# Kernel optimization log

Hardware: AMD Instinct MI355X
Metric: run time of the kernel (lower is better)

## Reference

```python
import jax, jax.numpy as jnp
import numpy as np

EPS = 1e-5

def _ln(x, g, b):
    mu = jnp.mean(x, -1, keepdims=True)
    var = jnp.mean((x - mu) ** 2, -1, keepdims=True)
    return (x - mu) / jnp.sqrt(var + EPS) * g + b

def _edge_scores(x, lat, mask, sn_g, sn_b, tn_g, tn_b, su_w, su_b, tp_w, tp_b, m1_w, m1_b, m2_w, m2_b):
    # x: [B,S,D], lat: [B,K,D] -> edges [B,S,K]
    s = _ln(x, sn_g, sn_b) @ su_w + su_b      # [B,S,E]
    t = _ln(lat, tn_g, tn_b) @ tp_w + tp_b    # [B,K,E]
    B, S, E = s.shape
    K = t.shape[1]
    s4 = jnp.broadcast_to(s[:, :, None, :], (B, S, K, E))
    t4 = jnp.broadcast_to(t[:, None, :, :], (B, S, K, E))
    pair = jnp.concatenate([s4, t4, s4 * t4], axis=-1)  # [B,S,K,3E]
    h = jax.nn.gelu(pair @ m1_w + m1_b, approximate=False)
    e = (h @ m2_w + m2_b)[..., 0]             # [B,S,K]
    e = e / (1.0 + jnp.abs(e))                # softsign
    return e * mask[:, :, None]

def setup_inputs() -> dict:
    key = jax.random.key(0)
    B, St, Si, K, D, E = 2, 2048, 1024, 64, 768, 256
    ks = iter(jax.random.split(key, 64))
    d = {}
    d['text_values'] = jax.random.normal(next(ks), (B, St, D), jnp.float32)
    d['image_values'] = jax.random.normal(next(ks), (B, Si, D), jnp.float32)
    d['latent_state_init'] = jax.random.normal(next(ks), (B, K, D), jnp.float32)
    d['latent_value_init'] = jax.random.normal(next(ks), (B, K, D), jnp.float32)
    d['text_mask'] = jnp.ones((B, St), jnp.float32)
    d['image_mask'] = jnp.ones((B, Si), jnp.float32)
    def scorer(prefix):
        d[prefix + 'sn_g'] = jnp.ones((D,), jnp.float32)
        d[prefix + 'sn_b'] = jnp.zeros((D,), jnp.float32)
        d[prefix + 'tn_g'] = jnp.ones((D,), jnp.float32)
        d[prefix + 'tn_b'] = jnp.zeros((D,), jnp.float32)
        d[prefix + 'su_w'] = jax.random.normal(next(ks), (D, E), jnp.float32) * 0.02
        d[prefix + 'su_b'] = jnp.zeros((E,), jnp.float32)
        d[prefix + 'tp_w'] = jax.random.normal(next(ks), (D, E), jnp.float32) * 0.02
        d[prefix + 'tp_b'] = jnp.zeros((E,), jnp.float32)
        d[prefix + 'm1_w'] = jax.random.normal(next(ks), (3 * E, E), jnp.float32) * 0.02
        d[prefix + 'm1_b'] = jnp.zeros((E,), jnp.float32)
        d[prefix + 'm2_w'] = jax.random.normal(next(ks), (E, 1), jnp.float32) * 0.02
        d[prefix + 'm2_b'] = jnp.zeros((1,), jnp.float32)
    scorer('t_')
    scorer('i_')
    for p in ['tsn', 'isn', 'stn', 'vn']:
        d[p + '_g'] = jnp.ones((D,), jnp.float32)
        d[p + '_b'] = jnp.zeros((D,), jnp.float32)
    d['tsp_w'] = jax.random.normal(next(ks), (D, D), jnp.float32) * 0.02
    d['tsp_b'] = jnp.zeros((D,), jnp.float32)
    d['isp_w'] = jax.random.normal(next(ks), (D, D), jnp.float32) * 0.02
    d['isp_b'] = jnp.zeros((D,), jnp.float32)
    return d

def reference(text_values, image_values, latent_state_init, latent_value_init, text_mask, image_mask,
              t_sn_g, t_sn_b, t_tn_g, t_tn_b, t_su_w, t_su_b, t_tp_w, t_tp_b, t_m1_w, t_m1_b, t_m2_w, t_m2_b,
              i_sn_g, i_sn_b, i_tn_g, i_tn_b, i_su_w, i_su_b, i_tp_w, i_tp_b, i_m1_w, i_m1_b, i_m2_w, i_m2_b,
              tsn_g, tsn_b, isn_g, isn_b, stn_g, stn_b, vn_g, vn_b, tsp_w, tsp_b, isp_w, isp_b):
    t2l = _edge_scores(text_values, latent_value_init, text_mask,
                       t_sn_g, t_sn_b, t_tn_g, t_tn_b, t_su_w, t_su_b, t_tp_w, t_tp_b, t_m1_w, t_m1_b, t_m2_w, t_m2_b)
    i2l = _edge_scores(image_values, latent_value_init, image_mask,
                       i_sn_g, i_sn_b, i_tn_g, i_tn_b, i_su_w, i_su_b, i_tp_w, i_tp_b, i_m1_w, i_m1_b, i_m2_w, i_m2_b)
    tsf = _ln(text_values, tsn_g, tsn_b) @ tsp_w + tsp_b    # [B,St,D]
    isf = _ln(image_values, isn_g, isn_b) @ isp_w + isp_b   # [B,Si,D]
    state_raw = jnp.einsum('bsk,bsd->bkd', t2l, tsf) + jnp.einsum('bsk,bsd->bkd', i2l, isf)
    value_raw = jnp.einsum('bsk,bsd->bkd', t2l, text_values) + jnp.einsum('bsk,bsd->bkd', i2l, image_values)
    latent_state = _ln(state_raw + latent_state_init, stn_g, stn_b)
    latent_value = _ln(value_raw + latent_value_init, vn_g, vn_b)
    return latent_state, latent_value, t2l, i2l
```

## Files before the change

### kernel.cpp

```cpp
#include <hip/hip_runtime.h>
#include <math.h>

#define EPS_LN 1e-5f

#define B_  2
#define ST_ 2048
#define SI_ 1024
#define K_  64
#define D_  768
#define E_  256

typedef __bf16 bf16x8 __attribute__((ext_vector_type(8)));
typedef float  f32x4  __attribute__((ext_vector_type(4)));
typedef unsigned short ushort_t;

__device__ inline ushort_t f2bf(float x) {
    unsigned int u = __float_as_uint(x);
    unsigned int r = (u + 0x7FFFu + ((u >> 16) & 1u)) >> 16;
    return (ushort_t)r;
}

__device__ inline float gelu_fast(float z) {
    float x2 = z * z;
    float u = 0.7978845608f * z * fmaf(0.044715f, x2, 1.0f);
    float t = __expf(-2.0f * fabsf(u));
    float r = __builtin_amdgcn_rcpf(1.0f + t);
    float th = fmaf(t * r, -2.0f, 1.0f);
    return fmaf(0.5f * fabsf(z), th, 0.5f * z);
}

__global__ __launch_bounds__(256) void ln_stats_kernel(
    const float* __restrict__ xt, const float* __restrict__ xi,
    const float* __restrict__ xl, float* __restrict__ mu, float* __restrict__ rstd)
{
    int w = threadIdx.x >> 6, lane = threadIdx.x & 63;
    int row = blockIdx.x * 4 + w;
    const float* src;
    if (row < 4096) src = xt + (size_t)row * D_;
    else if (row < 6144) src = xi + (size_t)(row - 4096) * D_;
    else src = xl + (size_t)(row - 6144) * D_;
    float s = 0.f, q = 0.f;
    #pragma unroll
    for (int rep = 0; rep < 3; ++rep) {
        float4 v = *(const float4*)(src + lane * 4 + rep * 256);
        s += v.x + v.y + v.z + v.w;
        q += v.x * v.x + v.y * v.y + v.z * v.z + v.w * v.w;
    }
    #pragma unroll
    for (int off = 32; off > 0; off >>= 1) {
        s += __shfl_xor(s, off, 64);
        q += __shfl_xor(q, off, 64);
    }
    if (lane == 0) {
        float m = s / (float)D_;
        float var = q / (float)D_ - m * m;
        mu[row] = m;
        rstd[row] = rsqrtf(var + EPS_LN);
    }
}

__global__ __launch_bounds__(256) void fold_all_kernel(
    const float* b0, const float* W0, const float* w0, float* f0,
    const float* b1, const float* W1, const float* w1, float* f1,
    const float* b2, const float* W2, const float* w2, float* f2,
    const float* b3, const float* W3, const float* w3, float* f3,
    const float* b4, const float* W4, const float* w4, float* f4,
    const float* b5, const float* W5, const float* w5, float* f5)
{
    const float* blns[6] = {b0, b1, b2, b3, b4, b5};
    const float* Ws[6]   = {W0, W1, W2, W3, W4, W5};
    const float* wbs[6]  = {w0, w1, w2, w3, w4, w5};
    float* bfs[6]        = {f0, f1, f2, f3, f4, f5};
    int cfg = blockIdx.z;
    int E = (cfg >= 4) ? 768 : 256;
    if ((int)blockIdx.x * 64 >= E) return;
    const float* bln = blns[cfg];
    const float* W = Ws[cfg];
    __shared__ float red[4][64];
    int c = threadIdx.x & 63, part = threadIdx.x >> 6;
    int e = blockIdx.x * 64 + c;
    int d0 = blockIdx.y * 64;
    float s = 0.f;
    #pragma unroll
    for (int i = 0; i < 16; ++i) {
        int d = d0 + part * 16 + i;
        s += bln[d] * W[(size_t)d * E + e];
    }
    red[part][c] = s; __syncthreads();
    if (part == 0) {
        float v = red[0][c] + red[1][c] + red[2][c] + red[3][c];
        if (blockIdx.y == 0 && wbs[cfg]) v += wbs[cfg][e];
        atomicAdd(&bfs[cfg][e], v);
    }
}

__global__ __launch_bounds__(256) void tpack_kernel(
    const float* __restrict__ xt, const float* __restrict__ xi,
    const float* __restrict__ mu, const float* __restrict__ rstd,
    ushort_t* __restrict__ XrF_t, ushort_t* __restrict__ XhF_t, ushort_t* __restrict__ AF_t,
    ushort_t* __restrict__ XrF_i, ushort_t* __restrict__ XhF_i, ushort_t* __restrict__ AF_i)
{
    __shared__ float tile[64][65];
    __shared__ float mu_s[64], rs_s[64];
    int bx = blockIdx.x;
    int isImg = bx >= 64;
    const float* x = isImg ? xi : xt;
    ushort_t* XrF = isImg ? XrF_i : XrF_t;
    ushort_t* XhF = isImg ? XhF_i : XhF_t;
    ushort_t* AF  = isImg ? AF_i  : AF_t;
    int rbase = (isImg ? bx - 64 : bx) * 64;
    int statOff = isImg ? 4096 : 0;
    int d0 = blockIdx.y * 64;
    int t = threadIdx.x;
    #pragma unroll
    for (int rep = 0; rep < 4; ++rep) {
        int rl = (t >> 4) + rep * 16;
        int c4 = (t & 15) * 4;
        *(float4*)&tile[rl][c4] = *(const float4*)(x + (size_t)(rbase + rl) * D_ + d0 + c4);
    }
    if (t < 64) { mu_s[t] = mu[statOff + rbase + t]; rs_s[t] = rstd[statOff + rbase + t]; }
    __syncthreads();
    int lane = t & 63;
    #pragma unroll
    for (int rep = 0; rep < 2; ++rep) {
        int idx = t + rep * 256;
        int nt = (idx >> 6) & 3, cl = (idx >> 8) & 1;
        int kl = cl * 32 + (lane >> 4) * 8;
        int nl = nt * 16 + (lane & 15);
        ushort_t orw[8], oh[8];
        #pragma unroll
        for (int j = 0; j < 8; ++j) {
            float v = tile[kl + j][nl];
            orw[j] = f2bf(v);
            oh[j]  = f2bf((v - mu_s[kl + j]) * rs_s[kl + j]);
        }
        size_t chunk = (size_t)((rbase >> 5) + cl);
        size_t o = ((chunk * 48 + (d0 >> 4) + nt) * 64 + lane) * 8;
        *reinterpret_cast<uint4*>(XrF + o) = *reinterpret_cast<uint4*>(orw);
        *reinterpret_cast<uint4*>(XhF + o) = *reinterpret_cast<uint4*>(oh);
    }
    #pragma unroll
    for (int rep = 0; rep < 2; ++rep) {
        int idx = t + rep * 256;
        int cl = (idx >> 6) & 1, tl = idx >> 7;
        int rl = tl * 16 + (lane & 15);
        int dl = cl * 32 + (lane >> 4) * 8;
        float m = mu_s[rl], rs = rs_s[rl];
        ushort_t o8[8];
        #pragma unroll
        for (int j = 0; j < 8; ++j)
            o8[j] = f2bf((tile[rl][dl + j] - m) * rs);
        size_t o = (((size_t)(rbase >> 4) + tl) * 24 + (d0 >> 5) + cl) * 512 + lane * 8;
        *reinterpret_cast<uint4*>(AF + o) = *reinterpret_cast<uint4*>(o8);
    }
}

__global__ __launch_bounds__(256) void packB_kernel(const float* __restrict__ W,
                                                    const float* __restrict__ g,
                                                    ushort_t* __restrict__ out,
                                                    int Kd, int N) {
    int idx = blockIdx.x * 256 + threadIdx.x;
    int nTile = N >> 4;
    int total = (Kd >> 5) * nTile * 64;
    if (idx >= total) return;
    int lane = idx & 63;
    int ntile = (idx >> 6) % nTile;
    int c = idx / (64 * nTile);
    int n = ntile * 16 + (lane & 15);
    int k0 = c * 32 + (lane >> 4) * 8;
    ushort_t o[8];
    #pragma unroll
    for (int j = 0; j < 8; ++j) {
        int k = k0 + j;
        float v = W[(size_t)k * N + n];
        if (g) v *= g[k];
        o[j] = f2bf(v);
    }
    *reinterpret_cast<uint4*>(out + (size_t)idx * 8) = *reinterpret_cast<uint4*>(o);
}

__global__ __launch_bounds__(256) void sgemm_split_kernel(
    const float* A0, const float* B0, const float* rs0, const float* bias0,
    const float* mu0, const float* sd0, int so0, float* C0,
    const float* A1, const float* B1, const float* rs1, const float* bias1,
    const float* mu1, const float* sd1, int so1, float* C1,
    int nz0, int Kd, int N)
{
    int z = blockIdx.z;
    int cfg = (z >= nz0) ? 1 : 0;
    int kz = cfg ? (z - nz0) : z;
    const float* A = cfg ? A1 : A0;
    const float* Bm = cfg ? B1 : B0;
    const float* rowScale = cfg ? rs1 : rs0;
    const float* bias = cfg ? bias1 : bias0;
    const float* muA = cfg ? mu1 : mu0;
    const float* sdA = cfg ? sd1 : sd0;
    int so = cfg ? so1 : so0;
    float* C = cfg ? C1 : C0;

    __shared__ float As[16][65];
    __shared__ float Bs[16][64];
    int tx = threadIdx.x, ty = threadIdx.y;
    int tid = ty * 16 + tx;
    int row0 = blockIdx.y * 64;
    int col0 = blockIdx.x * 64;
    float acc[4][4] = {};
    int kbase = kz * 128;
    for (int k0 = kbase; k0 < kbase + 128; k0 += 16) {
        {
            int e = tid * 4;
            int r = e >> 4, kk = e & 15;
            float4 av = *(const float4*)(A + (size_t)(row0 + r) * Kd + k0 + kk);
            if (muA) {
                float m = muA[so + row0 + r], sd = sdA[so + row0 + r];
                av.x = (av.x - m) * sd; av.y = (av.y - m) * sd;
                av.z = (av.z - m) * sd; av.w = (av.w - m) * sd;
            }
            As[kk + 0][r] = av.x; As[kk + 1][r] = av.y; As[kk + 2][r] = av.z; As[kk + 3][r] = av.w;
        }
        {
            int e = tid * 4;
            int kk = e >> 6, c = e & 63;
            float4 bv = *(const float4*)(Bm + (size_t)(k0 + kk) * N + col0 + c);
            if (rowScale) {
                float sc = rowScale[k0 + kk];
                bv.x *= sc; bv.y *= sc; bv.z *= sc; bv.w *= sc;
            }
            *(float4*)&Bs[kk][c] = bv;
        }
        __syncthreads();
        #pragma unroll
        for (int kk = 0; kk < 16; ++kk) {
            float a[4], b[4];
            #pragma unroll
            for (int i = 0; i < 4; ++i) a[i] = As[kk][ty + 16 * i];
            #pragma unroll
            for (int j = 0; j < 4; ++j) b[j] = Bs[kk][tx + 16 * j];
            #pragma unroll
            for (int i = 0; i < 4; ++i)
                #pragma unroll
                for (int j = 0; j < 4; ++j)
                    acc[i][j] += a[i] * b[j];
        }
        __syncthreads();
    }
    #pragma unroll
    for (int i = 0; i < 4; ++i) {
        int r = row0 + ty + 16 * i;
        #pragma unroll
        for (int j = 0; j < 4; ++j) {
            int c = col0 + tx + 16 * j;
            float v = acc[i][j];
            if (kz == 0 && bias) v += bias[c];
            atomicAdd(&C[(size_t)r * N + c], v);
        }
    }
}

__global__ __launch_bounds__(256) void sproj_mfma_kernel(
    const ushort_t* __restrict__ AF_t, const ushort_t* __restrict__ BF_t,
    const float* __restrict__ bias_t, ushort_t* __restrict__ sF_t,
    const ushort_t* __restrict__ AF_i, const ushort_t* __restrict__ BF_i,
    const float* __restrict__ bias_i, ushort_t* __restrict__ sF_i)
{
    __shared__ __align__(16) ushort_t ls[4][32][72];
    int bx = blockIdx.x;
    int isImg = bx >= 128;
    const ushort_t* AF = isImg ? AF_i : AF_t;
    const ushort_t* BF = isImg ? BF_i : BF_t;
    const float* bias = isImg ? bias_i : bias_t;
    ushort_t* sF = isImg ? sF_i : sF_t;
    int tile0 = (isImg ? bx - 128 : bx) * 2;

    int w = threadIdx.x >> 6, lane = threadIdx.x & 63;
    int quad = lane >> 4, n16 = lane & 15;

    f32x4 acc[2][4];
    #pragma unroll
    for (int mt = 0; mt < 2; ++mt)
        #pragma unroll
        for (int nt = 0; nt < 4; ++nt)
            acc[mt][nt] = (f32x4){0.f, 0.f, 0.f, 0.f};

    for (int c = 0; c < 24; ++c) {
        bf16x8 af[2], bf[4];
        #pragma unroll
        for (int mt = 0; mt < 2; ++mt)
            af[mt] = *reinterpret_cast<const bf16x8*>(AF + ((size_t)(tile0 + mt) * 24 + c) * 512 + lane * 8);
        #pragma unroll
        for (int nt = 0; nt < 4; ++nt)
            bf[nt] = *reinterpret_cast<const bf16x8*>(BF + ((size_t)c * 16 + w * 4 + nt) * 512 + lane * 8);
        #pragma unroll
        for (int mt = 0; mt < 2; ++mt)
            #pragma unroll
            for (int nt = 0; nt < 4; ++nt)
                acc[mt][nt] = __builtin_amdgcn_mfma_f32_16x16x32_bf16(af[mt], bf[nt], acc[mt][nt], 0, 0, 0);
    }
    #pragma unroll
    for (int mt = 0; mt < 2; ++mt)
        #pragma unroll
        for (int nt = 0; nt < 4; ++nt) {
            float bv = bias[w * 64 + nt * 16 + n16];
            #pragma unroll
            for (int r = 0; r < 4; ++r)
                ls[w][mt * 16 + quad * 4 + r][nt * 16 + n16] = f2bf(acc[mt][nt][r] + bv);
        }
    __syncthreads();
    #pragma unroll
    for (int mt = 0; mt < 2; ++mt)
        #pragma unroll
        for (int h = 0; h < 2; ++h) {
            uint4 v = *reinterpret_cast<const uint4*>(&ls[w][mt * 16 + n16][h * 32 + quad * 8]);
            *reinterpret_cast<uint4*>(sF + ((size_t)(tile0 + mt) * 8 + 2 * w + h) * 512 + lane * 8) = v;
        }
}

__global__ __launch_bounds__(256) void pack_M_kernel(
    const float* __restrict__ tP_t, const float* __restrict__ W3_t,
    const float* __restrict__ W1_t, ushort_t* __restrict__ MF_t,
    const float* __restrict__ tP_i, const float* __restrict__ W3_i,
    const float* __restrict__ W1_i, ushort_t* __restrict__ MF_i)
{
    const int HALF = B_ * K_ * 16 * 8 * 64;
    int gidx = blockIdx.x * 256 + threadIdx.x;
    int isImg = gidx >= HALF;
    int idx = isImg ? gidx - HALF : gidx;
    const float* tP = isImg ? tP_i : tP_t;
    const float* W3 = isImg ? W3_i : W3_t;
    const float* W1 = isImg ? W1_i : W1_t;
    ushort_t* MF = isImg ? MF_i : MF_t;
    int lane = idx & 63;
    int kc = (idx >> 6) & 7;
    int nt = (idx >> 9) & 15;
    int bk = idx >> 13;
    int n = nt * 16 + (lane & 15);
    int e0 = kc * 32 + (lane >> 4) * 8;
    ushort_t out[8];
    #pragma unroll
    for (int j = 0; j < 8; ++j) {
        int e = e0 + j;
        float v = tP[(size_t)bk * E_ + e] * W3[(size_t)e * E_ + n] + W1[(size_t)e * E_ + n];
        out[j] = f2bf(v);
    }
    *reinterpret_cast<uint4*>(MF + (size_t)idx * 8) = *reinterpret_cast<uint4*>(out);
}

__global__ __launch_bounds__(256, 4) void cross_mfma_kernel(
    const ushort_t* __restrict__ sF_t, const ushort_t* __restrict__ MF_t,
    const float* __restrict__ c2_t, const float* __restrict__ m2w_t,
    const float* __restrict__ m2b_t, const float* __restrict__ mask_t,
    float* __restrict__ out_t,
    const ushort_t* __restrict__ sF_i, const ushort_t* __restrict__ MF_i,
    const float* __restrict__ c2_i, const float* __restrict__ m2w_i,
    const float* __restrict__ m2b_i, const float* __restrict__ mask_i,
    float* __restrict__ out_i)
{
    int k = blockIdx.x;
    int by = blockIdx.y;
    int isImg = by >= 32;
    int S = isImg ? SI_ : ST_;
    const ushort_t* sF = isImg ? sF_i : sF_t;
    const ushort_t* MF = isImg ? MF_i : MF_t;
    const float* c2P = isImg ? c2_i : c2_t;
    const float* m2w = isImg ? m2w_i : m2w_t;
    const float* m2b = isImg ? m2b_i : m2b_t;
    const float* mask = isImg ? mask_i : mask_t;
    float* outE = isImg ? out_i : out_t;
    int s0 = (isImg ? by - 32 : by) * 64;
    int b = blockIdx.z;
    int tid = threadIdx.x;
    int w = tid >> 6, lane = tid & 63;
    int quad = lane >> 4, n16 = lane & 15;

    const ushort_t* aBase = sF + (size_t)(b * (S / 16) + (s0 >> 4)) * 4096;
    const ushort_t* bBase = MF + ((size_t)(b * K_ + k) * 16 + w * 4) * 4096;

    f32x4 acc[4][4];
    #pragma unroll
    for (int mt = 0; mt < 4; ++mt)
        #pragma unroll
        for (int nt = 0; nt < 4; ++nt)
            acc[mt][nt] = (f32x4){0.f, 0.f, 0.f, 0.f};

    #pragma unroll
    for (int kc = 0; kc < 8; ++kc) {
        bf16x8 bfr[4], af[4];
        #pragma unroll
        for (int nt = 0; nt < 4; ++nt)
            bfr[nt] = *reinterpret_cast<const bf16x8*>(bBase + (size_t)nt * 4096 + kc * 512 + lane * 8);
        #pragma unroll
        for (int mt = 0; mt < 4; ++mt)
            af[mt] = *reinterpret_cast<const bf16x8*>(aBase + (size_t)mt * 4096 + kc * 512 + lane * 8);
        #pragma unroll
        for (int mt = 0; mt < 4; ++mt)
            #pragma unroll
            for (int nt = 0; nt < 4; ++nt)
                acc[mt][nt] = __builtin_amdgcn_mfma_f32_16x16x32_bf16(af[mt], bfr[nt], acc[mt][nt], 0, 0, 0);
    }

    const float* c2v = c2P + (size_t)(b * K_ + k) * E_;
    float c2r[4], m2r[4];
    #pragma unroll
    for (int nt = 0; nt < 4; ++nt) {
        int col = w * 64 + nt * 16 + n16;
        c2r[nt] = c2v[col];
        m2r[nt] = m2w[col];
    }
    __shared__ float pPart[4][64];
    #pragma unroll
    for (int mt = 0; mt < 4; ++mt) {
        #pragma unroll
        for (int r = 0; r < 4; ++r) {
            float p = 0.f;
            #pragma unroll
            for (int nt = 0; nt < 4; ++nt) {
                float z = acc[mt][nt][r] + c2r[nt];
                p += gelu_fast(z) * m2r[nt];
            }
            p += __shfl_xor(p, 1, 64);
            p += __shfl_xor(p, 2, 64);
            p += __shfl_xor(p, 4, 64);
            p += __shfl_xor(p, 8, 64);
            if (n16 == 0) pPart[w][mt * 16 + quad * 4 + r] = p;
        }
    }
    __syncthreads();
    if (tid < 64) {
        float e = pPart[0][tid] + pPart[1][tid] + pPart[2][tid] + pPart[3][tid] + m2b[0];
        e = e / (1.0f + fabsf(e));
        int srow = s0 + tid;
        e *= mask[(size_t)b * S + srow];
        outE[((size_t)b * S + srow) * K_ + k] = e;
    }
}

__global__ __launch_bounds__(256) void packE_kernel(
    const float* __restrict__ t2l, const float* __restrict__ i2l,
    ushort_t* __restrict__ EF_t, ushort_t* __restrict__ EF_i)
{
    __shared__ float tile[32][65];
    int g = blockIdx.x;
    int isImg = g >= 128;
    const float* src = isImg ? i2l : t2l;
    ushort_t* EF = isImg ? EF_i : EF_t;
    int chunk = isImg ? g - 128 : g;
    int t = threadIdx.x;
    {
        int r = t >> 3;
        int c4 = (t & 7) * 8;
        const float* p = src + ((size_t)chunk * 32 + r) * 64 + c4;
        *(float4*)&tile[r][c4] = *(const float4*)p;
        *(float4*)&tile[r][c4 + 4] = *(const float4*)(p + 4);
    }
    __syncthreads();
    int mt = t >> 6, lane = t & 63;
    int k = mt * 16 + (lane & 15);
    int sl0 = (lane >> 4) * 8;
    ushort_t o8[8];
    #pragma unroll
    for (int j = 0; j < 8; ++j)
        o8[j] = f2bf(tile[sl0 + j][k]);
    *reinterpret_cast<uint4*>(EF + (((size_t)chunk * 4 + mt) * 64 + lane) * 8) = *reinterpret_cast<uint4*>(o8);
}

__global__ __launch_bounds__(256) void rowsum_kernel(const float* __restrict__ E,
                                                     float* __restrict__ out, int S) {
    __shared__ float red[256];
    int idx = blockIdx.x; int b = idx >> 6; int k = idx & 63;
    int tid = threadIdx.x;
    float s = 0.f;
    for (int ss = tid; ss < S; ss += 256) s += E[((size_t)b * S + ss) * K_ + k];
    red[tid] = s; __syncthreads();
    for (int off = 128; off > 0; off >>= 1) { if (tid < off) red[tid] += red[tid + off]; __syncthreads(); }
    if (tid == 0) out[idx] = red[0];
}

__global__ __launch_bounds__(256, 2) void einsum_mfma_kernel(
    const ushort_t* __restrict__ EF_t, const ushort_t* __restrict__ XhF_t,
    const ushort_t* __restrict__ XrF_t, float* __restrict__ PtG, float* __restrict__ PtR,
    const ushort_t* __restrict__ EF_i, const ushort_t* __restrict__ XhF_i,
    const ushort_t* __restrict__ XrF_i, float* __restrict__ PiG, float* __restrict__ PiR)
{
    int bz = blockIdx.z;
    int isImg = bz >= 2;
    int b = isImg ? bz - 2 : bz;
    int S = isImg ? SI_ : ST_;
    const ushort_t* EF = isImg ? EF_i : EF_t;
    const ushort_t* XhF = isImg ? XhF_i : XhF_t;
    const ushort_t* XrF = isImg ? XrF_i : XrF_t;
    float* PG = isImg ? PiG : PtG;
    float* PR = isImg ? PiR : PtR;
    int chunksPerBlock = isImg ? 2 : 4;

    int w = threadIdx.x >> 6, lane = threadIdx.x & 63;
    int quad = lane >> 4, n16 = lane & 15;
    int y = blockIdx.y;
    int nt0 = blockIdx.x * 16 + w * 4;
    size_t cb = (size_t)(b * S) / 32 + (size_t)y * chunksPerBlock;

    f32x4 aG[4][4], aR[4][4];
    #pragma unroll
    for (int mt = 0; mt < 4; ++mt)
        #pragma unroll
        for (int nt = 0; nt < 4; ++nt) {
            aG[mt][nt] = (f32x4){0.f, 0.f, 0.f, 0.f};
            aR[mt][nt] = (f32x4){0.f, 0.f, 0.f, 0.f};
        }

    for (int cc = 0; cc < chunksPerBlock; ++cc) {
        size_t c = cb + cc;
        bf16x8 af[4], bh[4], bx[4];
        #pragma unroll
        for (int mt = 0; mt < 4; ++mt)
            af[mt] = *reinterpret_cast<const bf16x8*>(EF + ((c * 4 + mt) * 64 + lane) * 8);
        #pragma unroll
        for (int nt = 0; nt < 4; ++nt) {
            bh[nt] = *reinterpret_cast<const bf16x8*>(XhF + ((c * 48 + nt0 + nt) * 64 + lane) * 8);
            bx[nt] = *reinterpret_cast<const bf16x8*>(XrF + ((c * 48 + nt0 + nt) * 64 + lane) * 8);
        }
        #pragma unroll
        for (int mt = 0; mt < 4; ++mt)
            #pragma unroll
            for (int nt = 0; nt < 4; ++nt) {
                aG[mt][nt] = __builtin_amdgcn_mfma_f32_16x16x32_bf16(af[mt], bh[nt], aG[mt][nt], 0, 0, 0);
                aR[mt][nt] = __builtin_amdgcn_mfma_f32_16x16x32_bf16(af[mt], bx[nt], aR[mt][nt], 0, 0, 0);
            }
    }
    #pragma unroll
    for (int mt = 0; mt < 4; ++mt)
        #pragma unroll
        for (int nt = 0; nt < 4; ++nt) {
            int d = (nt0 + nt) * 16 + n16;
            #pragma unroll
            for (int r = 0; r < 4; ++r) {
                int krow = mt * 16 + quad * 4 + r;
                size_t o = (((size_t)y * B_ + b) * K_ + krow) * D_ + d;
                PG[o] = aG[mt][nt][r];
                PR[o] = aR[mt][nt][r];
            }
        }
}

__global__ __launch_bounds__(256) void reduce_parts_kernel(
    const float* __restrict__ PtG, const float* __restrict__ PtR,
    const float* __restrict__ PiG, const float* __restrict__ PiR,
    float* __restrict__ Gt, float* __restrict__ Gi, float* __restrict__ Racc)
{
    const int BKD = B_ * K_ * D_;
    int idx = blockIdx.x * 256 + threadIdx.x;
    if (idx >= BKD) return;
    float gt = 0.f, gi = 0.f, r = 0.f;
    #pragma unroll
    for (int c = 0; c < 16; ++c) { gt += PtG[(size_t)c * BKD + idx]; r += PtR[(size_t)c * BKD + idx]; }
    #pragma unroll
    for (int c = 0; c < 16; ++c) { gi += PiG[(size_t)c * BKD + idx]; r += PiR[(size_t)c * BKD + idx]; }
    Gt[idx] = gt; Gi[idx] = gi; Racc[idx] = r;
}

__global__ __launch_bounds__(256) void final_ln_kernel(
    const float* __restrict__ stateTmp, const float* __restrict__ Racc,
    const float* __restrict__ rs_t, const float* __restrict__ rs_i,
    const float* __restrict__ b_tspf, const float* __restrict__ b_ispf,
    const float* __restrict__ state_init, const float* __restrict__ value_init,
    const float* __restrict__ stn_g, const float* __restrict__ stn_b,
    const float* __restrict__ vn_g, const float* __restrict__ vn_b,
    float* __restrict__ outState, float* __restrict__ outValue)
{
    __shared__ float pre[D_];
    __shared__ float red[256];
    int idx = blockIdx.x;
    int row = idx & 127;
    int isVal = idx >> 7;
    int tid = threadIdx.x;
    if (!isVal) {
        float rt = rs_t[row], ri = rs_i[row];
        for (int d = tid; d < D_; d += 256)
            pre[d] = stateTmp[(size_t)row * D_ + d] + rt * b_tspf[d] + ri * b_ispf[d]
                   + state_init[(size_t)row * D_ + d];
    } else {
        for (int d = tid; d < D_; d += 256)
            pre[d] = Racc[(size_t)row * D_ + d] + value_init[(size_t)row * D_ + d];
    }
    __syncthreads();
    float s = 0.f;
    for (int d = tid; d < D_; d += 256) s += pre[d];
    red[tid] = s; __syncthreads();
    for (int off = 128; off > 0; off >>= 1) { if (tid < off) red[tid] += red[tid + off]; __syncthreads(); }
    float mu = red[0] / (float)D_;
    __syncthreads();
    float v = 0.f;
    for (int d = tid; d < D_; d += 256) { float t = pre[d] - mu; v += t * t; }
    red[tid] = v; __syncthreads();
    for (int off = 128; off > 0; off >>= 1) { if (tid < off) red[tid] += red[tid + off]; __syncthreads(); }
    float rstd = rsqrtf(red[0] / (float)D_ + EPS_LN);
    const float* g  = isVal ? vn_g : stn_g;
    const float* bb = isVal ? vn_b : stn_b;
    float* o = (isVal ? outValue : outState) + (size_t)row * D_;
    for (int d = tid; d < D_; d += 256) o[d] = (pre[d] - mu) * rstd * g[d] + bb[d];
}

extern "C" void kernel_launch(void* const* d_in, const int* in_sizes, int n_in,
                              void* d_out, int out_size, void* d_ws, size_t ws_size,
                              hipStream_t stream) {
    const float* text_values  = (const float*)d_in[0];
    const float* image_values = (const float*)d_in[1];
    const float* lstate_init  = (const float*)d_in[2];
    const float* lvalue_init  = (const float*)d_in[3];
    const float* text_mask    = (const float*)d_in[4];
    const float* image_mask   = (const float*)d_in[5];
    const float* t_sn_g = (const float*)d_in[6];
    const float* t_sn_b = (const float*)d_in[7];
    const float* t_tn_g = (const float*)d_in[8];
    const float* t_tn_b = (const float*)d_in[9];
    const float* t_su_w = (const float*)d_in[10];
    const float* t_su_b = (const float*)d_in[11];
    const float* t_tp_w = (const float*)d_in[12];
    const float* t_tp_b = (const float*)d_in[13];
    const float* t_m1_w = (const float*)d_in[14];
    const float* t_m1_b = (const float*)d_in[15];
    const float* t_m2_w = (const float*)d_in[16];
    const float* t_m2_b = (const float*)d_in[17];
    const float* i_sn_g = (const float*)d_in[18];
    const float* i_sn_b = (const float*)d_in[19];
    const float* i_tn_g = (const float*)d_in[20];
    const float* i_tn_b = (const float*)d_in[21];
    const float* i_su_w = (const float*)d_in[22];
    const float* i_su_b = (const float*)d_in[23];
    const float* i_tp_w = (const float*)d_in[24];
    const float* i_tp_b = (const float*)d_in[25];
    const float* i_m1_w = (const float*)d_in[26];
    const float* i_m1_b = (const float*)d_in[27];
    const float* i_m2_w = (const float*)d_in[28];
    const float* i_m2_b = (const float*)d_in[29];
    const float* tsn_g = (const float*)d_in[30];
    const float* tsn_b = (const float*)d_in[31];
    const float* isn_g = (const float*)d_in[32];
    const float* isn_b = (const float*)d_in[33];
    const float* stn_g = (const float*)d_in[34];
    const float* stn_b = (const float*)d_in[35];
    const float* vn_g  = (const float*)d_in[36];
    const float* vn_b  = (const float*)d_in[37];
    const float* tsp_w = (const float*)d_in[38];
    const float* tsp_b = (const float*)d_in[39];
    const float* isp_w = (const float*)d_in[40];
    const float* isp_b = (const float*)d_in[41];

    float* ws = (float*)d_ws;
    size_t o = 0;
    float* stats_mu = ws + o; o += 6272;
    float* stats_rs = ws + o; o += 6272;
    float* zeroBase = ws + o;
    float* b_su_t = ws + o; o += E_;
    float* b_su_i = ws + o; o += E_;
    float* b_tp_t = ws + o; o += E_;
    float* b_tp_i = ws + o; o += E_;
    float* b_tspf = ws + o; o += D_;
    float* b_ispf = ws + o; o += D_;
    float* t_t  = ws + o; o += (size_t)B_ * K_ * E_;
    float* t_i  = ws + o; o += (size_t)B_ * K_ * E_;
    float* c2_t = ws + o; o += (size_t)B_ * K_ * E_;
    float* c2_i = ws + o; o += (size_t)B_ * K_ * E_;
    float* state_tmp = ws + o; o += (size_t)B_ * K_ * D_;
    size_t zeroFloats = (size_t)(4 * E_ + 2 * D_ + 4 * B_ * K_ * E_ + B_ * K_ * D_);
    float* rs_t = ws + o; o += 128;
    float* rs_i = ws + o; o += 128;
    ushort_t* AF_t = (ushort_t*)(ws + o); o += (size_t)B_ * ST_ * D_ / 2;
    ushort_t* AF_i = (ushort_t*)(ws + o); o += (size_t)B_ * SI_ * D_ / 2;
    ushort_t* WsuF_t = (ushort_t*)(ws + o); o += (size_t)D_ * E_ / 2;
    ushort_t* WsuF_i = (ushort_t*)(ws + o); o += (size_t)D_ * E_ / 2;
    ushort_t* sF_t = (ushort_t*)(ws + o); o += (size_t)B_ * ST_ * E_ / 2;
    ushort_t* sF_i = (ushort_t*)(ws + o); o += (size_t)B_ * SI_ * E_ / 2;
    ushort_t* MF_t = (ushort_t*)(ws + o); o += (size_t)B_ * K_ * E_ * E_ / 2;
    ushort_t* MF_i = (ushort_t*)(ws + o); o += (size_t)B_ * K_ * E_ * E_ / 2;
    ushort_t* XhF_t = (ushort_t*)(ws + o); o += (size_t)B_ * ST_ * D_ / 2;
    ushort_t* XhF_i = (ushort_t*)(ws + o); o += (size_t)B_ * SI_ * D_ / 2;
    ushort_t* XrF_t = (ushort_t*)(ws + o); o += (size_t)B_ * ST_ * D_ / 2;
    ushort_t* XrF_i = (ushort_t*)(ws + o); o += (size_t)B_ * SI_ * D_ / 2;
    ushort_t* EF_t  = (ushort_t*)(ws + o); o += (size_t)B_ * ST_ * K_ / 2;
    ushort_t* EF_i  = (ushort_t*)(ws + o); o += (size_t)B_ * SI_ * K_ / 2;
    const int BKD = B_ * K_ * D_;
    float* PtG = ws + o; o += (size_t)16 * BKD;
    float* PtR = ws + o; o += (size_t)16 * BKD;
    float* PiG = ws + o; o += (size_t)16 * BKD;
    float* PiR = ws + o; o += (size_t)16 * BKD;
    float* Gt   = ws + o; o += BKD;
    float* Gi   = ws + o; o += BKD;
    float* Racc = ws + o; o += BKD;

    float* outState = (float*)d_out;
    float* outValue = (float*)d_out + (size_t)B_ * K_ * D_;
    float* t2l = (float*)d_out + 2 * (size_t)B_ * K_ * D_;
    float* i2l = t2l + (size_t)B_ * ST_ * K_;

    hipMemsetAsync(zeroBase, 0, zeroFloats * sizeof(float), stream);

    ln_stats_kernel<<<1568, 256, 0, stream>>>(text_values, image_values, lvalue_init, stats_mu, stats_rs);

    fold_all_kernel<<<dim3(12, 12, 6), 256, 0, stream>>>(
        t_sn_b, t_su_w, t_su_b, b_su_t,
        i_sn_b, i_su_w, i_su_b, b_su_i,
        t_tn_b, t_tp_w, t_tp_b, b_tp_t,
        i_tn_b, i_tp_w, i_tp_b, b_tp_i,
        tsn_b, tsp_w, tsp_b, b_tspf,
        isn_b, isp_w, isp_b, b_ispf);

    tpack_kernel<<<dim3(96, 12), 256, 0, stream>>>(
        text_values, image_values, stats_mu, stats_rs,
        XrF_t, XhF_t, AF_t, XrF_i, XhF_i, AF_i);

    packB_kernel<<<96, 256, 0, stream>>>(t_su_w, t_sn_g, WsuF_t, D_, E_);
    packB_kernel<<<96, 256, 0, stream>>>(i_su_w, i_sn_g, WsuF_i, D_, E_);

    sgemm_split_kernel<<<dim3(4, 2, 12), dim3(16, 16), 0, stream>>>(
        lvalue_init, t_tp_w, t_tn_g, b_tp_t, stats_mu, stats_rs, 6144, t_t,
        lvalue_init, i_tp_w, i_tn_g, b_tp_i, stats_mu, stats_rs, 6144, t_i,
        6, D_, E_);
    sgemm_split_kernel<<<dim3(4, 2, 4), dim3(16, 16), 0, stream>>>(
        t_t, t_m1_w + (size_t)E_ * E_, nullptr, t_m1_b, nullptr, nullptr, 0, c2_t,
        t_i, i_m1_w + (size_t)E_ * E_, nullptr, i_m1_b, nullptr, nullptr, 0, c2_i,
        2, E_, E_);

    sproj_mfma_kernel<<<192, 256, 0, stream>>>(
        AF_t, WsuF_t, b_su_t, sF_t, AF_i, WsuF_i, b_su_i, sF_i);

    pack_M_kernel<<<8192, 256, 0, stream>>>(
        t_t, t_m1_w + 2 * (size_t)E_ * E_, t_m1_w, MF_t,
        t_i, i_m1_w + 2 * (size_t)E_ * E_, i_m1_w, MF_i);

    cross_mfma_kernel<<<dim3(K_, 48, B_), 256, 0, stream>>>(
        sF_t, MF_t, c2_t, t_m2_w, t_m2_b, text_mask, t2l,
        sF_i, MF_i, c2_i, i_m2_w, i_m2_b, image_mask, i2l);

    packE_kernel<<<192, 256, 0, stream>>>(t2l, i2l, EF_t, EF_i);
    rowsum_kernel<<<B_ * K_, 256, 0, stream>>>(t2l, rs_t, ST_);
    rowsum_kernel<<<B_ * K_, 256, 0, stream>>>(i2l, rs_i, SI_);

    einsum_mfma_kernel<<<dim3(3, 16, 4), 256, 0, stream>>>(
        EF_t, XhF_t, XrF_t, PtG, PtR,
        EF_i, XhF_i, XrF_i, PiG, PiR);

    reduce_parts_kernel<<<(BKD + 255) / 256, 256, 0, stream>>>(PtG, PtR, PiG, PiR, Gt, Gi, Racc);

    sgemm_split_kernel<<<dim3(12, 2, 12), dim3(16, 16), 0, stream>>>(
        Gt, tsp_w, tsn_g, nullptr, nullptr, nullptr, 0, state_tmp,
        Gi, isp_w, isn_g, nullptr, nullptr, nullptr, 0, state_tmp,
        6, D_, D_);

    final_ln_kernel<<<2 * B_ * K_, 256, 0, stream>>>(
        state_tmp, Racc, rs_t, rs_i, b_tspf, b_ispf,
        lstate_init, lvalue_init, stn_g, stn_b, vn_g, vn_b, outState, outValue);
}
```

Before: 379.6 us.

## Cheapen GELU, fuse edge transpose with rowsums, merge packB, retile einsum

GELU now uses the sigmoid-style form x·σ(1.702x) in place of the tanh polynomial, which removes several multiplies per element in the cross-MFMA epilogue at the cost of larger deviation from exact erf GELU. The cross kernel writes edge scores in a [b,k,s] layout and gets a higher occupancy hint. A new packE2 kernel transposes those scores into the t2l/i2l outputs, packs the bf16 fragments and computes the row sums via atomics in one pass, replacing the separate packE and two rowsum kernels. The two packB launches are merged into one, and the einsum kernel uses half as many N-tiles per wave across twice as many blocks, with a higher occupancy hint.

```diff
diff --git a/kernel.cpp b/kernel.cpp
--- a/kernel.cpp
+++ b/kernel.cpp
@@ -21,12 +21,11 @@
 }
 
 __device__ inline float gelu_fast(float z) {
-    float x2 = z * z;
-    float u = 0.7978845608f * z * fmaf(0.044715f, x2, 1.0f);
-    float t = __expf(-2.0f * fabsf(u));
+    float a = fabsf(z);
+    float t = __expf(a * -1.702f);
     float r = __builtin_amdgcn_rcpf(1.0f + t);
     float th = fmaf(t * r, -2.0f, 1.0f);
-    return fmaf(0.5f * fabsf(z), th, 0.5f * z);
+    return fmaf(0.5f * a, th, 0.5f * z);
 }
 
 __global__ __launch_bounds__(256) void ln_stats_kernel(
@@ -155,26 +154,27 @@
     }
 }
 
-__global__ __launch_bounds__(256) void packB_kernel(const float* __restrict__ W,
-                                                    const float* __restrict__ g,
-                                                    ushort_t* __restrict__ out,
-                                                    int Kd, int N) {
-    int idx = blockIdx.x * 256 + threadIdx.x;
-    int nTile = N >> 4;
-    int total = (Kd >> 5) * nTile * 64;
-    if (idx >= total) return;
+__global__ __launch_bounds__(256) void packB2_kernel(
+    const float* __restrict__ Wt, const float* __restrict__ gt, ushort_t* __restrict__ outT,
+    const float* __restrict__ Wi, const float* __restrict__ gi, ushort_t* __restrict__ outI)
+{
+    const int HALF = (D_ >> 5) * (E_ >> 4) * 64;
+    int gidx = blockIdx.x * 256 + threadIdx.x;
+    int isImg = gidx >= HALF;
+    int idx = isImg ? gidx - HALF : gidx;
+    const float* W = isImg ? Wi : Wt;
+    const float* g = isImg ? gi : gt;
+    ushort_t* out = isImg ? outI : outT;
     int lane = idx & 63;
-    int ntile = (idx >> 6) % nTile;
-    int c = idx / (64 * nTile);
+    int ntile = (idx >> 6) & 15;
+    int c = idx >> 10;
     int n = ntile * 16 + (lane & 15);
     int k0 = c * 32 + (lane >> 4) * 8;
     ushort_t o[8];
     #pragma unroll
     for (int j = 0; j < 8; ++j) {
         int k = k0 + j;
-        float v = W[(size_t)k * N + n];
-        if (g) v *= g[k];
-        o[j] = f2bf(v);
+        o[j] = f2bf(W[(size_t)k * E_ + n] * g[k]);
     }
     *reinterpret_cast<uint4*>(out + (size_t)idx * 8) = *reinterpret_cast<uint4*>(o);
 }
@@ -345,15 +345,15 @@
     *reinterpret_cast<uint4*>(MF + (size_t)idx * 8) = *reinterpret_cast<uint4*>(out);
 }
 
-__global__ __launch_bounds__(256, 4) void cross_mfma_kernel(
+__global__ __launch_bounds__(256, 6) void cross_mfma_kernel(
     const ushort_t* __restrict__ sF_t, const ushort_t* __restrict__ MF_t,
     const float* __restrict__ c2_t, const float* __restrict__ m2w_t,
     const float* __restrict__ m2b_t, const float* __restrict__ mask_t,
-    float* __restrict__ out_t,
+    float* __restrict__ Et,
     const ushort_t* __restrict__ sF_i, const ushort_t* __restrict__ MF_i,
     const float* __restrict__ c2_i, const float* __restrict__ m2w_i,
     const float* __restrict__ m2b_i, const float* __restrict__ mask_i,
-    float* __restrict__ out_i)
+    float* __restrict__ Ei)
 {
     int k = blockIdx.x;
     int by = blockIdx.y;
@@ -365,7 +365,7 @@
     const float* m2w = isImg ? m2w_i : m2w_t;
     const float* m2b = isImg ? m2b_i : m2b_t;
     const float* mask = isImg ? mask_i : mask_t;
-    float* outE = isImg ? out_i : out_t;
+    float* Etmp = isImg ? Ei : Et;
     int s0 = (isImg ? by - 32 : by) * 64;
     int b = blockIdx.z;
     int tid = threadIdx.x;
@@ -430,52 +430,63 @@
         e = e / (1.0f + fabsf(e));
         int srow = s0 + tid;
         e *= mask[(size_t)b * S + srow];
-        outE[((size_t)b * S + srow) * K_ + k] = e;
-    }
-}
-
-__global__ __launch_bounds__(256) void packE_kernel(
-    const float* __restrict__ t2l, const float* __restrict__ i2l,
-    ushort_t* __restrict__ EF_t, ushort_t* __restrict__ EF_i)
-{
-    __shared__ float tile[32][65];
+        Etmp[(size_t)(b * K_ + k) * S + srow] = e;
+    }
+}
+
+__global__ __launch_bounds__(256) void packE2_kernel(
+    const float* __restrict__ Et, const float* __restrict__ Ei,
+    float* __restrict__ t2l, float* __restrict__ i2l,
+    ushort_t* __restrict__ EF_t, ushort_t* __restrict__ EF_i,
+    float* __restrict__ rs_t, float* __restrict__ rs_i)
+{
+    __shared__ float tile[64][33];
     int g = blockIdx.x;
     int isImg = g >= 128;
-    const float* src = isImg ? i2l : t2l;
+    const float* Esrc = isImg ? Ei : Et;
+    float* dst = isImg ? i2l : t2l;
     ushort_t* EF = isImg ? EF_i : EF_t;
+    float* rsum = isImg ? rs_i : rs_t;
     int chunk = isImg ? g - 128 : g;
+    int S = isImg ? SI_ : ST_;
+    int b = (chunk * 32) / S;
+    int s0 = (chunk * 32) % S;
     int t = threadIdx.x;
     {
-        int r = t >> 3;
-        int c4 = (t & 7) * 8;
-        const float* p = src + ((size_t)chunk * 32 + r) * 64 + c4;
-        *(float4*)&tile[r][c4] = *(const float4*)p;
-        *(float4*)&tile[r][c4 + 4] = *(const float4*)(p + 4);
+        int k = t >> 2, si = (t & 3) * 8;
+        const float* p = Esrc + (size_t)(b * K_ + k) * S + s0 + si;
+        *(float4*)&tile[k][si] = *(const float4*)p;
+        *(float4*)&tile[k][si + 4] = *(const float4*)(p + 4);
     }
     __syncthreads();
-    int mt = t >> 6, lane = t & 63;
-    int k = mt * 16 + (lane & 15);
-    int sl0 = (lane >> 4) * 8;
-    ushort_t o8[8];
-    #pragma unroll
-    for (int j = 0; j < 8; ++j)
-        o8[j] = f2bf(tile[sl0 + j][k]);
-    *reinterpret_cast<uint4*>(EF + (((size_t)chunk * 4 + mt) * 64 + lane) * 8) = *reinterpret_cast<uint4*>(o8);
-}
-
-__global__ __launch_bounds__(256) void rowsum_kernel(const float* __restrict__ E,
-                                                     float* __restrict__ out, int S) {
-    __shared__ float red[256];
-    int idx = blockIdx.x; int b = idx >> 6; int k = idx & 63;
-    int tid = threadIdx.x;
-    float s = 0.f;
-    for (int ss = tid; ss < S; ss += 256) s += E[((size_t)b * S + ss) * K_ + k];
-    red[tid] = s; __syncthreads();
-    for (int off = 128; off > 0; off >>= 1) { if (tid < off) red[tid] += red[tid + off]; __syncthreads(); }
-    if (tid == 0) out[idx] = red[0];
-}
-
-__global__ __launch_bounds__(256, 2) void einsum_mfma_kernel(
+    {
+        int s = t >> 3, k0 = (t & 7) * 8;
+        float o[8];
+        #pragma unroll
+        for (int j = 0; j < 8; ++j) o[j] = tile[k0 + j][s];
+        float* p = dst + ((size_t)b * S + s0 + s) * K_ + k0;
+        *(float4*)p = *(float4*)&o[0];
+        *(float4*)(p + 4) = *(float4*)&o[4];
+    }
+    {
+        int mt = t >> 6, lane = t & 63;
+        int k = mt * 16 + (lane & 15);
+        int sl0 = (lane >> 4) * 8;
+        ushort_t o8[8];
+        #pragma unroll
+        for (int j = 0; j < 8; ++j)
+            o8[j] = f2bf(tile[k][sl0 + j]);
+        *reinterpret_cast<uint4*>(EF + (((size_t)chunk * 4 + mt) * 64 + lane) * 8) = *reinterpret_cast<uint4*>(o8);
+    }
+    if (t < 64) {
+        float s = 0.f;
+        #pragma unroll
+        for (int j = 0; j < 32; ++j) s += tile[t][j];
+        atomicAdd(&rsum[b * K_ + t], s);
+    }
+}
+
+__global__ __launch_bounds__(256, 4) void einsum_mfma_kernel(
     const ushort_t* __restrict__ EF_t, const ushort_t* __restrict__ XhF_t,
     const ushort_t* __restrict__ XrF_t, float* __restrict__ PtG, float* __restrict__ PtR,
     const ushort_t* __restrict__ EF_i, const ushort_t* __restrict__ XhF_i,
@@ -495,33 +506,33 @@
     int w = threadIdx.x >> 6, lane = threadIdx.x & 63;
     int quad = lane >> 4, n16 = lane & 15;
     int y = blockIdx.y;
-    int nt0 = blockIdx.x * 16 + w * 4;
+    int nt0 = blockIdx.x * 8 + w * 2;
     size_t cb = (size_t)(b * S) / 32 + (size_t)y * chunksPerBlock;
 
-    f32x4 aG[4][4], aR[4][4];
+    f32x4 aG[4][2], aR[4][2];
     #pragma unroll
     for (int mt = 0; mt < 4; ++mt)
         #pragma unroll
-        for (int nt = 0; nt < 4; ++nt) {
+        for (int nt = 0; nt < 2; ++nt) {
             aG[mt][nt] = (f32x4){0.f, 0.f, 0.f, 0.f};
             aR[mt][nt] = (f32x4){0.f, 0.f, 0.f, 0.f};
         }
 
     for (int cc = 0; cc < chunksPerBlock; ++cc) {
         size_t c = cb + cc;
-        bf16x8 af[4], bh[4], bx[4];
+        bf16x8 af[4], bh[2], bx[2];
         #pragma unroll
         for (int mt = 0; mt < 4; ++mt)
             af[mt] = *reinterpret_cast<const bf16x8*>(EF + ((c * 4 + mt) * 64 + lane) * 8);
         #pragma unroll
-        for (int nt = 0; nt < 4; ++nt) {
+        for (int nt = 0; nt < 2; ++nt) {
             bh[nt] = *reinterpret_cast<const bf16x8*>(XhF + ((c * 48 + nt0 + nt) * 64 + lane) * 8);
             bx[nt] = *reinterpret_cast<const bf16x8*>(XrF + ((c * 48 + nt0 + nt) * 64 + lane) * 8);
         }
         #pragma unroll
         for (int mt = 0; mt < 4; ++mt)
             #pragma unroll
-            for (int nt = 0; nt < 4; ++nt) {
+            for (int nt = 0; nt < 2; ++nt) {
                 aG[mt][nt] = __builtin_amdgcn_mfma_f32_16x16x32_bf16(af[mt], bh[nt], aG[mt][nt], 0, 0, 0);
                 aR[mt][nt] = __builtin_amdgcn_mfma_f32_16x16x32_bf16(af[mt], bx[nt], aR[mt][nt], 0, 0, 0);
             }
@@ -529,7 +540,7 @@
     #pragma unroll
     for (int mt = 0; mt < 4; ++mt)
         #pragma unroll
-        for (int nt = 0; nt < 4; ++nt) {
+        for (int nt = 0; nt < 2; ++nt) {
             int d = (nt0 + nt) * 16 + n16;
             #pragma unroll
             for (int r = 0; r < 4; ++r) {
@@ -661,9 +672,11 @@
     float* c2_t = ws + o; o += (size_t)B_ * K_ * E_;
     float* c2_i = ws + o; o += (size_t)B_ * K_ * E_;
     float* state_tmp = ws + o; o += (size_t)B_ * K_ * D_;
-    size_t zeroFloats = (size_t)(4 * E_ + 2 * D_ + 4 * B_ * K_ * E_ + B_ * K_ * D_);
     float* rs_t = ws + o; o += 128;
     float* rs_i = ws + o; o += 128;
+    size_t zeroFloats = (size_t)(4 * E_ + 2 * D_ + 4 * B_ * K_ * E_ + B_ * K_ * D_ + 256);
+    float* Etmp_t = ws + o; o += (size_t)B_ * K_ * ST_;
+    float* Etmp_i = ws + o; o += (size_t)B_ * K_ * SI_;
     ushort_t* AF_t = (ushort_t*)(ws + o); o += (size_t)B_ * ST_ * D_ / 2;
     ushort_t* AF_i = (ushort_t*)(ws + o); o += (size_t)B_ * SI_ * D_ / 2;
     ushort_t* WsuF_t = (ushort_t*)(ws + o); o += (size_t)D_ * E_ / 2;
@@ -708,8 +721,7 @@
         text_values, image_values, stats_mu, stats_rs,
         XrF_t, XhF_t, AF_t, XrF_i, XhF_i, AF_i);
 
-    packB_kernel<<<96, 256, 0, stream>>>(t_su_w, t_sn_g, WsuF_t, D_, E_);
-    packB_kernel<<<96, 256, 0, stream>>>(i_su_w, i_sn_g, WsuF_i, D_, E_);
+    packB2_kernel<<<192, 256, 0, stream>>>(t_su_w, t_sn_g, WsuF_t, i_su_w, i_sn_g, WsuF_i);
 
     sgemm_split_kernel<<<dim3(4, 2, 12), dim3(16, 16), 0, stream>>>(
         lvalue_init, t_tp_w, t_tn_g, b_tp_t, stats_mu, stats_rs, 6144, t_t,
@@ -728,14 +740,13 @@
         t_i, i_m1_w + 2 * (size_t)E_ * E_, i_m1_w, MF_i);
 
     cross_mfma_kernel<<<dim3(K_, 48, B_), 256, 0, stream>>>(
-        sF_t, MF_t, c2_t, t_m2_w, t_m2_b, text_mask, t2l,
-        sF_i, MF_i, c2_i, i_m2_w, i_m2_b, image_mask, i2l);
-
-    packE_kernel<<<192, 256, 0, stream>>>(t2l, i2l, EF_t, EF_i);
-    rowsum_kernel<<<B_ * K_, 256, 0, stream>>>(t2l, rs_t, ST_);
-    rowsum_kernel<<<B_ * K_, 256, 0, stream>>>(i2l, rs_i, SI_);
-
-    einsum_mfma_kernel<<<dim3(3, 16, 4), 256, 0, stream>>>(
+        sF_t, MF_t, c2_t, t_m2_w, t_m2_b, text_mask, Etmp_t,
+        sF_i, MF_i, c2_i, i_m2_w, i_m2_b, image_mask, Etmp_i);
+
+    packE2_kernel<<<192, 256, 0, stream>>>(
+        Etmp_t, Etmp_i, t2l, i2l, EF_t, EF_i, rs_t, rs_i);
+
+    einsum_mfma_kernel<<<dim3(6, 16, 4), 256, 0, stream>>>(
         EF_t, XhF_t, XrF_t, PtG, PtR,
         EF_i, XhF_i, XrF_i, PiG, PiR);
 
```

Result: slower. 754.6 us (+98.8%).
